# Kernel tuning notes

Hardware: AMD Instinct MI355X
Metric: run time of the kernel (lower is better)

Reference implementation:

```python
import jax, jax.numpy as jnp
import numpy as np

N_NODES = 100000
N_EDGES = 1600000
IN_F, HID, N_COLORS = 128, 128, 10


def setup_inputs() -> dict:
    key = jax.random.key(0)
    k1, k2, k3, k4 = jax.random.split(key, 4)
    x = jax.random.normal(k1, (N_NODES, IN_F), dtype=jnp.float32)
    edge_index = jax.random.randint(k2, (2, N_EDGES), 0, N_NODES, dtype=jnp.int64)
    # Glorot-ish init for weights
    W1 = jax.random.normal(k3, (IN_F, HID), dtype=jnp.float32) / np.sqrt(IN_F)
    b1 = jnp.zeros((HID,), dtype=jnp.float32)
    W2 = jax.random.normal(k4, (HID, N_COLORS), dtype=jnp.float32) / np.sqrt(HID)
    b2 = jnp.zeros((N_COLORS,), dtype=jnp.float32)
    return {"x": x, "edge_index": edge_index, "W1": W1, "b1": b1, "W2": W2, "b2": b2}


def _gcn_norm(edge_index, num_nodes):
    # Add self-loops, compute symmetric normalization D^-1/2 (A+I) D^-1/2
    loops = jnp.arange(num_nodes, dtype=edge_index.dtype)
    src = jnp.concatenate([edge_index[0], loops])
    dst = jnp.concatenate([edge_index[1], loops])
    deg = jax.ops.segment_sum(jnp.ones_like(dst, dtype=jnp.float32), dst,
                              num_segments=num_nodes)
    deg_isqrt = jax.lax.rsqrt(deg)  # deg >= 1 due to self-loops
    norm = deg_isqrt[src] * deg_isqrt[dst]  # [E + N]
    return src, dst, norm


def _gcn_conv(h, src, dst, norm, num_nodes, W, b):
    # Linear transform first (PyG GCNConv), then gather-scale-scatter aggregate
    h = h @ W                                   # [N, out]
    msg = h[src] * norm[:, None]                # [E + N, out] gather
    out = jax.ops.segment_sum(msg, dst, num_segments=num_nodes)  # scatter-add
    return out + b


def reference(x, edge_index, W1, b1, W2, b2):
    n = x.shape[0]
    src, dst, norm = _gcn_norm(edge_index, n)
    h = _gcn_conv(x, src, dst, norm, n, W1, b1)
    h = jax.nn.relu(h)
    # dropout is identity in eval mode
    h = _gcn_conv(h, src, dst, norm, n, W2, b2)
    return jax.nn.softmax(h, axis=1)
```

## Files before the change

### kernel.cpp

```cpp
#include <hip/hip_runtime.h>
#include <hip/hip_fp16.h>

#define IN_F 128
#define HID  128
#define NC   10
#define H2P  16
#define NPB  128
#define NBMAX 784
#define BCAP 2560
#define EPB  4096

typedef _Float16 f16x8 __attribute__((ext_vector_type(8)));
typedef float f32x4 __attribute__((ext_vector_type(4)));
typedef int int4a __attribute__((ext_vector_type(4), aligned(4)));

__device__ inline __half2 shfl_xor_h2(__half2 v, int mask) {
    int i = __shfl_xor(*reinterpret_cast<int*>(&v), mask, 64);
    return *reinterpret_cast<__half2*>(&i);
}

__global__ __launch_bounds__(1024) void k_bin(const int* __restrict__ src,
                                              const int* __restrict__ dst,
                                              int* __restrict__ bcnt,
                                              unsigned int* __restrict__ binned,
                                              const float* __restrict__ W1,
                                              __half* __restrict__ WT,
                                              int E, int nbin) {
    __shared__ int hist[NBMAX];
    __shared__ int base[NBMAX];
    __shared__ int lcur[NBMAX];
    const int tid = threadIdx.x;

    if (blockIdx.x == 0) {
        for (int i = tid; i < IN_F * HID; i += 1024) {
            int k = i >> 7, n = i & 127;
            WT[n * IN_F + k] = __float2half(W1[k * HID + n]);
        }
    }

    for (int b = tid; b < nbin; b += 1024) { hist[b] = 0; lcur[b] = 0; }
    __syncthreads();

    const int e0 = blockIdx.x * EPB + tid;
    int d[4];
    #pragma unroll
    for (int u = 0; u < 4; u++) {
        int e = e0 + u * 1024;
        d[u] = (e < E) ? dst[e] : -1;
        if (d[u] >= 0) atomicAdd(&hist[d[u] >> 7], 1);
    }
    __syncthreads();
    for (int b = tid; b < nbin; b += 1024) {
        int h = hist[b];
        base[b] = h ? atomicAdd(&bcnt[b], h) : 0;
    }
    __syncthreads();
    #pragma unroll
    for (int u = 0; u < 4; u++) {
        int e = e0 + u * 1024;
        if (e < E) {
            int dd = d[u];
            int b = dd >> 7;
            int s = src[e];
            int o = base[b] + atomicAdd(&lcur[b], 1);
            if (o < BCAP)
                binned[(size_t)b * BCAP + o] = ((unsigned)(dd & 127) << 17) | (unsigned)s;
        }
    }
}

__global__ __launch_bounds__(256) void k_place2(const int* __restrict__ bcnt,
                                                const unsigned int* __restrict__ binned,
                                                int* __restrict__ rowptr,
                                                float* __restrict__ dis,
                                                int* __restrict__ csr,
                                                int N, int E, int nbin) {
    __shared__ int h[NPB];
    __shared__ int lb[NPB];
    __shared__ int cur[NPB];
    __shared__ int red[256];
    const int b = blockIdx.x;
    const int tid = threadIdx.x;

    int partial = 0;
    for (int i = tid; i < b; i += 256) partial += bcnt[i];
    red[tid] = partial;
    if (tid < NPB) h[tid] = 0;
    __syncthreads();
    #pragma unroll
    for (int off = 128; off > 0; off >>= 1) {
        if (tid < off) red[tid] += red[tid + off];
        __syncthreads();
    }
    const int rb = red[0];

    const int m = min(bcnt[b], BCAP);
    const unsigned int* p = binned + (size_t)b * BCAP;
    for (int i = tid; i < m; i += 256) atomicAdd(&h[p[i] >> 17], 1);
    __syncthreads();
    if (tid < NPB) lb[tid] = h[tid];
    __syncthreads();
    #pragma unroll
    for (int off = 1; off < NPB; off <<= 1) {
        int t = (tid < NPB && tid >= off) ? lb[tid - off] : 0;
        __syncthreads();
        if (tid < NPB) lb[tid] += t;
        __syncthreads();
    }
    if (tid < NPB) {
        int ex = lb[tid] - h[tid];
        int node = b * NPB + tid;
        if (node < N) {
            rowptr[node] = rb + ex;
            dis[node] = rsqrtf(1.0f + (float)h[tid]);
        }
        lb[tid] = ex;
        cur[tid] = 0;
    }
    if (b == nbin - 1 && tid == 0) rowptr[N] = E;
    __syncthreads();
    for (int i = tid; i < m; i += 256) {
        unsigned v = p[i];
        int dl = v >> 17;
        int r = atomicAdd(&cur[dl], 1);
        csr[rb + lb[dl] + r] = (int)(v & 0x1FFFF);
    }
}

__global__ __launch_bounds__(256) void k_gemm1(const float* __restrict__ X,
                                               const __half* __restrict__ WT,
                                               const float* __restrict__ dis,
                                               __half* __restrict__ outh) {
    __shared__ _Float16 sX[32 * IN_F];
    __shared__ _Float16 sW[128 * IN_F];
    const int tid = threadIdx.x;
    const int row0 = blockIdx.x * 32;

    {
        int n = tid >> 1, part = tid & 1;
        const f16x8* src = (const f16x8*)(WT + n * IN_F + part * 64);
        f16x8* dst = (f16x8*)(sW + n * IN_F + part * 64);
        #pragma unroll
        for (int c = 0; c < 8; c++) dst[c] = src[c];
    }
    {
        int r = tid >> 3;
        int k0 = (tid & 7) * 16;
        const float* sp = X + (size_t)(row0 + r) * IN_F + k0;
        float4 f0 = *(const float4*)(sp);
        float4 f1 = *(const float4*)(sp + 4);
        float4 f2 = *(const float4*)(sp + 8);
        float4 f3 = *(const float4*)(sp + 12);
        f16x8 h0, h1;
        h0[0] = (_Float16)f0.x; h0[1] = (_Float16)f0.y;
        h0[2] = (_Float16)f0.z; h0[3] = (_Float16)f0.w;
        h0[4] = (_Float16)f1.x; h0[5] = (_Float16)f1.y;
        h0[6] = (_Float16)f1.z; h0[7] = (_Float16)f1.w;
        h1[0] = (_Float16)f2.x; h1[1] = (_Float16)f2.y;
        h1[2] = (_Float16)f2.z; h1[3] = (_Float16)f2.w;
        h1[4] = (_Float16)f3.x; h1[5] = (_Float16)f3.y;
        h1[6] = (_Float16)f3.z; h1[7] = (_Float16)f3.w;
        *(f16x8*)(sX + r * IN_F + k0) = h0;
        *(f16x8*)(sX + r * IN_F + k0 + 8) = h1;
    }
    __syncthreads();

    const int wave = tid >> 6;
    const int lane = tid & 63;
    const int quad = lane >> 4;
    const int l16 = lane & 15;
    const int nbase = wave * 32;

    f32x4 acc00 = {0,0,0,0}, acc01 = {0,0,0,0}, acc10 = {0,0,0,0}, acc11 = {0,0,0,0};

    #pragma unroll
    for (int kc = 0; kc < 4; kc++) {
        const int koff = kc * 32 + quad * 8;
        f16x8 a0 = *(const f16x8*)(sX + l16 * IN_F + koff);
        f16x8 a1 = *(const f16x8*)(sX + (16 + l16) * IN_F + koff);
        f16x8 b0 = *(const f16x8*)(sW + (nbase + l16) * IN_F + koff);
        f16x8 b1 = *(const f16x8*)(sW + (nbase + 16 + l16) * IN_F + koff);
        acc00 = __builtin_amdgcn_mfma_f32_16x16x32_f16(a0, b0, acc00, 0, 0, 0);
        acc01 = __builtin_amdgcn_mfma_f32_16x16x32_f16(a0, b1, acc01, 0, 0, 0);
        acc10 = __builtin_amdgcn_mfma_f32_16x16x32_f16(a1, b0, acc10, 0, 0, 0);
        acc11 = __builtin_amdgcn_mfma_f32_16x16x32_f16(a1, b1, acc11, 0, 0, 0);
    }

    #pragma unroll
    for (int r = 0; r < 4; r++) {
        {
            int row = row0 + quad * 4 + r;
            float d = dis[row];
            __half* o = outh + (size_t)row * HID + nbase + l16;
            o[0]  = __float2half(acc00[r] * d);
            o[16] = __float2half(acc01[r] * d);
        }
        {
            int row = row0 + 16 + quad * 4 + r;
            float d = dis[row];
            __half* o = outh + (size_t)row * HID + nbase + l16;
            o[0]  = __float2half(acc10[r] * d);
            o[16] = __float2half(acc11[r] * d);
        }
    }
}

__global__ __launch_bounds__(256) void k_agg1(const __half* __restrict__ hsh,
                                              const int* __restrict__ rowptr,
                                              const int* __restrict__ csr,
                                              const float* __restrict__ dis,
                                              const float* __restrict__ b1,
                                              const float* __restrict__ W2,
                                              __half* __restrict__ h2h,
                                              int N, int E) {
    __shared__ float sWT[NC][IN_F];
    for (int i = threadIdx.x; i < NC * IN_F; i += 256)
        sWT[i >> 7][i & 127] = W2[(i & 127) * NC + (i >> 7)];
    __syncthreads();

    const int node = blockIdx.x * 4 + (threadIdx.x >> 6);
    if (node >= N) return;
    const int lane = threadIdx.x & 63;
    const int g   = lane >> 4;
    const int l16 = lane & 15;
    const int f0  = l16 * 8;

    const int beg = rowptr[node], end = rowptr[node + 1];
    const __half2 hz = __half2half2(__float2half(0.0f));
    const __half2 ho = __half2half2(__float2half(1.0f));
    const unsigned nclamp = (unsigned)(N - 1);

    __half2 acc2[4] = {hz, hz, hz, hz};
    if (g == 0) {
        float4 r = *(const float4*)(hsh + (size_t)node * HID + f0);
        const __half2* hh = (const __half2*)&r;
        acc2[0] = hh[0]; acc2[1] = hh[1]; acc2[2] = hh[2]; acc2[3] = hh[3];
    }

    for (int j0 = beg + 4 * g; j0 < end; j0 += 16) {
        int bj = min(j0, E - 4);
        int off = j0 - bj;
        int rem = end - j0;
        int4a cv = *(const int4a*)(csr + bj);
        unsigned s0 = min((unsigned)cv[0], nclamp);
        unsigned s1 = min((unsigned)cv[1], nclamp);
        unsigned s2 = min((unsigned)cv[2], nclamp);
        unsigned s3 = min((unsigned)cv[3], nclamp);
        __half2 w0 = ((unsigned)(0 - off) < (unsigned)rem) ? ho : hz;
        __half2 w1 = ((unsigned)(1 - off) < (unsigned)rem) ? ho : hz;
        __half2 w2 = ((unsigned)(2 - off) < (unsigned)rem) ? ho : hz;
        __half2 w3 = ((unsigned)(3 - off) < (unsigned)rem) ? ho : hz;
        float4 r0 = *(const float4*)(hsh + (size_t)s0 * HID + f0);
        float4 r1 = *(const float4*)(hsh + (size_t)s1 * HID + f0);
        float4 r2 = *(const float4*)(hsh + (size_t)s2 * HID + f0);
        float4 r3 = *(const float4*)(hsh + (size_t)s3 * HID + f0);
        const __half2* h0 = (const __half2*)&r0;
        const __half2* h1 = (const __half2*)&r1;
        const __half2* h2 = (const __half2*)&r2;
        const __half2* h3 = (const __half2*)&r3;
        #pragma unroll
        for (int i = 0; i < 4; i++) {
            acc2[i] = __hfma2(w0, h0[i], acc2[i]);
            acc2[i] = __hfma2(w1, h1[i], acc2[i]);
            acc2[i] = __hfma2(w2, h2[i], acc2[i]);
            acc2[i] = __hfma2(w3, h3[i], acc2[i]);
        }
    }

    #pragma unroll
    for (int i = 0; i < 4; i++) {
        acc2[i] = __hadd2(acc2[i], shfl_xor_h2(acc2[i], 16));
        acc2[i] = __hadd2(acc2[i], shfl_xor_h2(acc2[i], 32));
    }
    float acc[8];
    #pragma unroll
    for (int i = 0; i < 4; i++) {
        float2 t = __half22float2(acc2[i]);
        acc[2 * i] = t.x; acc[2 * i + 1] = t.y;
    }

    const float d = dis[node];
    float4 ba = *(const float4*)(b1 + f0);
    float4 bb = *(const float4*)(b1 + f0 + 4);
    float h[8];
    h[0] = fmaxf(fmaf(d, acc[0], ba.x), 0.0f);
    h[1] = fmaxf(fmaf(d, acc[1], ba.y), 0.0f);
    h[2] = fmaxf(fmaf(d, acc[2], ba.z), 0.0f);
    h[3] = fmaxf(fmaf(d, acc[3], ba.w), 0.0f);
    h[4] = fmaxf(fmaf(d, acc[4], bb.x), 0.0f);
    h[5] = fmaxf(fmaf(d, acc[5], bb.y), 0.0f);
    h[6] = fmaxf(fmaf(d, acc[6], bb.z), 0.0f);
    h[7] = fmaxf(fmaf(d, acc[7], bb.w), 0.0f);

    const int cb = (g == 0) ? 0 : (g == 1) ? 3 : (g == 2) ? 6 : 8;
    const int nc = (g < 2) ? 3 : 2;
    float p[3];
    #pragma unroll
    for (int ci = 0; ci < 3; ci++) {
        if (ci < nc) {
            int c = cb + ci;
            float4 wa = *(const float4*)&sWT[c][f0];
            float4 wb = *(const float4*)&sWT[c][f0 + 4];
            float t = fmaf(h[0], wa.x, fmaf(h[1], wa.y, fmaf(h[2], wa.z, h[3] * wa.w)));
            t = fmaf(h[4], wb.x, fmaf(h[5], wb.y, fmaf(h[6], wb.z, fmaf(h[7], wb.w, t))));
            #pragma unroll
            for (int off = 1; off < 16; off <<= 1) t += __shfl_xor(t, off, 64);
            p[ci] = t;
        }
    }
    if (l16 == 0) {
        __half* o = h2h + (size_t)node * H2P + cb;
        for (int ci = 0; ci < nc; ci++) o[ci] = __float2half(d * p[ci]);
    }
}

__global__ __launch_bounds__(256) void k_agg2(const __half* __restrict__ h2h,
                                              const int* __restrict__ rowptr,
                                              const int* __restrict__ csr,
                                              const float* __restrict__ dis,
                                              const float* __restrict__ b2,
                                              float* __restrict__ out,
                                              int N, int E) {
    int t = blockIdx.x * 256 + threadIdx.x;
    int node = t >> 1;
    int q = t & 1;
    if (node >= N) return;
    const int base = q * 8;
    const __half2 hz = __half2half2(__float2half(0.0f));
    const __half2 ho = __half2half2(__float2half(1.0f));
    const unsigned nclamp = (unsigned)(N - 1);

    __half2 a2[4];
    {
        float4 r = *(const float4*)(h2h + (size_t)node * H2P + base);
        const __half2* hh = (const __half2*)&r;
        a2[0] = hh[0]; a2[1] = hh[1]; a2[2] = hh[2]; a2[3] = hh[3];
    }
    const int beg = rowptr[node], end = rowptr[node + 1];
    for (int j0 = beg; j0 < end; j0 += 4) {
        int bj = min(j0, E - 4);
        int off = j0 - bj;
        int rem = end - j0;
        int4a cv = *(const int4a*)(csr + bj);
        unsigned s0 = min((unsigned)cv[0], nclamp);
        unsigned s1 = min((unsigned)cv[1], nclamp);
        unsigned s2 = min((unsigned)cv[2], nclamp);
        unsigned s3 = min((unsigned)cv[3], nclamp);
        __half2 w0 = ((unsigned)(0 - off) < (unsigned)rem) ? ho : hz;
        __half2 w1 = ((unsigned)(1 - off) < (unsigned)rem) ? ho : hz;
        __half2 w2 = ((unsigned)(2 - off) < (unsigned)rem) ? ho : hz;
        __half2 w3 = ((unsigned)(3 - off) < (unsigned)rem) ? ho : hz;
        float4 r0 = *(const float4*)(h2h + (size_t)s0 * H2P + base);
        float4 r1 = *(const float4*)(h2h + (size_t)s1 * H2P + base);
        float4 r2 = *(const float4*)(h2h + (size_t)s2 * H2P + base);
        float4 r3 = *(const float4*)(h2h + (size_t)s3 * H2P + base);
        const __half2* h0 = (const __half2*)&r0;
        const __half2* h1 = (const __half2*)&r1;
        const __half2* h2 = (const __half2*)&r2;
        const __half2* h3 = (const __half2*)&r3;
        #pragma unroll
        for (int i = 0; i < 4; i++) {
            a2[i] = __hfma2(w0, h0[i], a2[i]);
            a2[i] = __hfma2(w1, h1[i], a2[i]);
            a2[i] = __hfma2(w2, h2[i], a2[i]);
            a2[i] = __hfma2(w3, h3[i], a2[i]);
        }
    }

    float a[8];
    #pragma unroll
    for (int i = 0; i < 4; i++) {
        float2 tt = __half22float2(a2[i]);
        a[2 * i] = tt.x; a[2 * i + 1] = tt.y;
    }

    const float d = dis[node];
    float vv[8];
    #pragma unroll
    for (int i = 0; i < 8; i++) {
        int f = base + i;
        vv[i] = (f < NC) ? fmaf(d, a[i], b2[f]) : -1e30f;
    }
    float m = vv[0];
    #pragma unroll
    for (int i = 1; i < 8; i++) m = fmaxf(m, vv[i]);
    m = fmaxf(m, __shfl_xor(m, 1, 64));
    float e[8];
    float s = 0.0f;
    #pragma unroll
    for (int i = 0; i < 8; i++) { e[i] = (base + i < NC) ? expf(vv[i] - m) : 0.0f; s += e[i]; }
    s += __shfl_xor(s, 1, 64);
    float inv = 1.0f / s;

    float* o = out + (size_t)node * NC;
    if (q == 0) {
        *(float2*)(o + 0) = make_float2(e[0] * inv, e[1] * inv);
        *(float2*)(o + 2) = make_float2(e[2] * inv, e[3] * inv);
        *(float2*)(o + 4) = make_float2(e[4] * inv, e[5] * inv);
        *(float2*)(o + 6) = make_float2(e[6] * inv, e[7] * inv);
    } else {
        *(float2*)(o + 8) = make_float2(e[0] * inv, e[1] * inv);
    }
}

extern "C" void kernel_launch(void* const* d_in, const int* in_sizes, int n_in,
                              void* d_out, int out_size, void* d_ws, size_t ws_size,
                              hipStream_t stream) {
    const float* x  = (const float*)d_in[0];
    const int*   ei = (const int*)d_in[1];
    const float* W1 = (const float*)d_in[2];
    const float* b1 = (const float*)d_in[3];
    const float* W2 = (const float*)d_in[4];
    const float* b2 = (const float*)d_in[5];
    float* out = (float*)d_out;

    const int N = in_sizes[0] / IN_F;
    const int E = in_sizes[1] / 2;
    const int* esrc = ei;
    const int* edst = ei + E;
    const int nbin = (N + NPB - 1) / NPB;

    char* ws = (char*)d_ws;
    int*    rowptr  = (int*)(ws);
    float*  dis     = (float*)(ws + 0x80000);
    int*    bcnt    = (int*)(ws + 0x100000);
    __half* WT      = (__half*)(ws + 0x110000);
    unsigned int* binned = (unsigned int*)(ws + 0x140000);
    int*    csr     = (int*)(ws + 0x940000);
    __half* hsh     = (__half*)(ws + 0x1040000);
    __half* h2h     = (__half*)(ws + 0x2A00000);

    hipMemsetAsync(bcnt, 0, (size_t)nbin * sizeof(int), stream);

    k_bin   <<<(E + EPB - 1) / EPB, 1024, 0, stream>>>(esrc, edst, bcnt, binned, W1, WT, E, nbin);
    k_place2<<<nbin, 256, 0, stream>>>(bcnt, binned, rowptr, dis, csr, N, E, nbin);
    k_gemm1 <<<N / 32, 256, 0, stream>>>(x, WT, dis, hsh);
    k_agg1  <<<(N + 3) / 4, 256, 0, stream>>>(hsh, rowptr, csr, dis, b1, W2, h2h, N, E);
    k_agg2  <<<(int)(((size_t)N * 2 + 255) / 256), 256, 0, stream>>>(h2h, rowptr, csr, dis, b2, out, N, E);
}
```

Before: 252.0 us.

## Fuse CSR placement with GEMM1, pad rows to multiples of four, parallelize agg2

The CSR placement kernel and the first GEMM are merged into one kernel per 128-node bin, which removes a launch and the serial per-block prefix sum over bin counts. Each node's edge list is padded to a multiple of four with a dummy index that points to a zeroed row, stored at fixed per-bin offsets (CAPP) and described by a (start, count) pair. This lets both aggregation loops drop the boundary masking and index clamping and use plain adds. W2 is transposed once up front, and agg2 now uses 8 threads per node with a shuffle reduction instead of 2. The fused kernel has much larger shared memory and fewer blocks, and the padding plus fixed bin capacity add slightly more gather traffic and a layout assumption about per-bin edge counts.

```diff
diff --git a/kernel.cpp b/kernel.cpp
--- a/kernel.cpp
+++ b/kernel.cpp
@@ -8,6 +8,7 @@
 #define NPB  128
 #define NBMAX 784
 #define BCAP 2560
+#define CAPP 2944
 #define EPB  4096
 
 typedef _Float16 f16x8 __attribute__((ext_vector_type(8)));
@@ -25,6 +26,8 @@
                                               unsigned int* __restrict__ binned,
                                               const float* __restrict__ W1,
                                               __half* __restrict__ WT,
+                                              const float* __restrict__ W2,
+                                              float* __restrict__ W2T,
                                               int E, int nbin) {
     __shared__ int hist[NBMAX];
     __shared__ int base[NBMAX];
@@ -36,6 +39,8 @@
             int k = i >> 7, n = i & 127;
             WT[n * IN_F + k] = __float2half(W1[k * HID + n]);
         }
+        for (int i = tid; i < NC * IN_F; i += 1024)
+            W2T[i] = W2[(i & 127) * NC + (i >> 7)];
     }
 
     for (int b = tid; b < nbin; b += 1024) { hist[b] = 0; lcur[b] = 0; }
@@ -69,36 +74,35 @@
     }
 }
 
-__global__ __launch_bounds__(256) void k_place2(const int* __restrict__ bcnt,
-                                                const unsigned int* __restrict__ binned,
-                                                int* __restrict__ rowptr,
-                                                float* __restrict__ dis,
-                                                int* __restrict__ csr,
-                                                int N, int E, int nbin) {
+__global__ __launch_bounds__(256) void k_pg(const int* __restrict__ bcnt,
+                                            const unsigned int* __restrict__ binned,
+                                            int2* __restrict__ rowinfo,
+                                            float* __restrict__ dis,
+                                            int* __restrict__ csr,
+                                            const float* __restrict__ X,
+                                            const __half* __restrict__ WT,
+                                            __half* __restrict__ hsh,
+                                            __half* __restrict__ h2h,
+                                            int N) {
     __shared__ int h[NPB];
     __shared__ int lb[NPB];
     __shared__ int cur[NPB];
-    __shared__ int red[256];
+    __shared__ float sdis[NPB];
+    __shared__ _Float16 sX[32 * IN_F];
+    __shared__ _Float16 sW[128 * IN_F];
     const int b = blockIdx.x;
     const int tid = threadIdx.x;
 
-    int partial = 0;
-    for (int i = tid; i < b; i += 256) partial += bcnt[i];
-    red[tid] = partial;
     if (tid < NPB) h[tid] = 0;
     __syncthreads();
-    #pragma unroll
-    for (int off = 128; off > 0; off >>= 1) {
-        if (tid < off) red[tid] += red[tid + off];
-        __syncthreads();
-    }
-    const int rb = red[0];
 
     const int m = min(bcnt[b], BCAP);
     const unsigned int* p = binned + (size_t)b * BCAP;
     for (int i = tid; i < m; i += 256) atomicAdd(&h[p[i] >> 17], 1);
     __syncthreads();
-    if (tid < NPB) lb[tid] = h[tid];
+
+    int myh = 0, cnt4 = 0;
+    if (tid < NPB) { myh = h[tid]; cnt4 = (myh + 3) & ~3; lb[tid] = cnt4; }
     __syncthreads();
     #pragma unroll
     for (int off = 1; off < NPB; off <<= 1) {
@@ -107,115 +111,118 @@
         if (tid < NPB) lb[tid] += t;
         __syncthreads();
     }
+    int ex = 0;
     if (tid < NPB) {
-        int ex = lb[tid] - h[tid];
+        ex = lb[tid] - cnt4;
         int node = b * NPB + tid;
         if (node < N) {
-            rowptr[node] = rb + ex;
-            dis[node] = rsqrtf(1.0f + (float)h[tid]);
+            rowinfo[node] = make_int2(b * CAPP + ex, cnt4);
+            float dd = rsqrtf(1.0f + (float)myh);
+            dis[node] = dd;
+            sdis[tid] = dd;
         }
         lb[tid] = ex;
         cur[tid] = 0;
     }
-    if (b == nbin - 1 && tid == 0) rowptr[N] = E;
     __syncthreads();
     for (int i = tid; i < m; i += 256) {
         unsigned v = p[i];
         int dl = v >> 17;
         int r = atomicAdd(&cur[dl], 1);
-        csr[rb + lb[dl] + r] = (int)(v & 0x1FFFF);
-    }
-}
-
-__global__ __launch_bounds__(256) void k_gemm1(const float* __restrict__ X,
-                                               const __half* __restrict__ WT,
-                                               const float* __restrict__ dis,
-                                               __half* __restrict__ outh) {
-    __shared__ _Float16 sX[32 * IN_F];
-    __shared__ _Float16 sW[128 * IN_F];
-    const int tid = threadIdx.x;
-    const int row0 = blockIdx.x * 32;
+        csr[b * CAPP + lb[dl] + r] = (int)(v & 0x1FFFF);
+    }
+    if (tid < NPB) {
+        for (int k = myh; k < cnt4; k++) csr[b * CAPP + ex + k] = N;
+    }
+    if (b == 0) {
+        f16x8 z = {0, 0, 0, 0, 0, 0, 0, 0};
+        if (tid < 16) *(f16x8*)(hsh + (size_t)N * HID + tid * 8) = z;
+        if (tid < 2)  *(f16x8*)(h2h + (size_t)N * H2P + tid * 8) = z;
+    }
 
     {
         int n = tid >> 1, part = tid & 1;
-        const f16x8* src = (const f16x8*)(WT + n * IN_F + part * 64);
-        f16x8* dst = (f16x8*)(sW + n * IN_F + part * 64);
+        const f16x8* srcp = (const f16x8*)(WT + n * IN_F + part * 64);
+        f16x8* dstp = (f16x8*)(sW + n * IN_F + part * 64);
         #pragma unroll
-        for (int c = 0; c < 8; c++) dst[c] = src[c];
-    }
-    {
-        int r = tid >> 3;
-        int k0 = (tid & 7) * 16;
-        const float* sp = X + (size_t)(row0 + r) * IN_F + k0;
-        float4 f0 = *(const float4*)(sp);
-        float4 f1 = *(const float4*)(sp + 4);
-        float4 f2 = *(const float4*)(sp + 8);
-        float4 f3 = *(const float4*)(sp + 12);
-        f16x8 h0, h1;
-        h0[0] = (_Float16)f0.x; h0[1] = (_Float16)f0.y;
-        h0[2] = (_Float16)f0.z; h0[3] = (_Float16)f0.w;
-        h0[4] = (_Float16)f1.x; h0[5] = (_Float16)f1.y;
-        h0[6] = (_Float16)f1.z; h0[7] = (_Float16)f1.w;
-        h1[0] = (_Float16)f2.x; h1[1] = (_Float16)f2.y;
-        h1[2] = (_Float16)f2.z; h1[3] = (_Float16)f2.w;
-        h1[4] = (_Float16)f3.x; h1[5] = (_Float16)f3.y;
-        h1[6] = (_Float16)f3.z; h1[7] = (_Float16)f3.w;
-        *(f16x8*)(sX + r * IN_F + k0) = h0;
-        *(f16x8*)(sX + r * IN_F + k0 + 8) = h1;
-    }
-    __syncthreads();
-
+        for (int c = 0; c < 8; c++) dstp[c] = srcp[c];
+    }
     const int wave = tid >> 6;
     const int lane = tid & 63;
     const int quad = lane >> 4;
     const int l16 = lane & 15;
     const int nbase = wave * 32;
 
-    f32x4 acc00 = {0,0,0,0}, acc01 = {0,0,0,0}, acc10 = {0,0,0,0}, acc11 = {0,0,0,0};
-
-    #pragma unroll
-    for (int kc = 0; kc < 4; kc++) {
-        const int koff = kc * 32 + quad * 8;
-        f16x8 a0 = *(const f16x8*)(sX + l16 * IN_F + koff);
-        f16x8 a1 = *(const f16x8*)(sX + (16 + l16) * IN_F + koff);
-        f16x8 b0 = *(const f16x8*)(sW + (nbase + l16) * IN_F + koff);
-        f16x8 b1 = *(const f16x8*)(sW + (nbase + 16 + l16) * IN_F + koff);
-        acc00 = __builtin_amdgcn_mfma_f32_16x16x32_f16(a0, b0, acc00, 0, 0, 0);
-        acc01 = __builtin_amdgcn_mfma_f32_16x16x32_f16(a0, b1, acc01, 0, 0, 0);
-        acc10 = __builtin_amdgcn_mfma_f32_16x16x32_f16(a1, b0, acc10, 0, 0, 0);
-        acc11 = __builtin_amdgcn_mfma_f32_16x16x32_f16(a1, b1, acc11, 0, 0, 0);
-    }
-
-    #pragma unroll
-    for (int r = 0; r < 4; r++) {
+    for (int tdx = 0; tdx < 4; tdx++) {
+        int row0 = b * NPB + tdx * 32;
+        if (row0 >= N) break;
+        __syncthreads();
         {
-            int row = row0 + quad * 4 + r;
-            float d = dis[row];
-            __half* o = outh + (size_t)row * HID + nbase + l16;
-            o[0]  = __float2half(acc00[r] * d);
-            o[16] = __float2half(acc01[r] * d);
-        }
-        {
-            int row = row0 + 16 + quad * 4 + r;
-            float d = dis[row];
-            __half* o = outh + (size_t)row * HID + nbase + l16;
-            o[0]  = __float2half(acc10[r] * d);
-            o[16] = __float2half(acc11[r] * d);
+            int r = tid >> 3;
+            int k0 = (tid & 7) * 16;
+            const float* sp = X + (size_t)(row0 + r) * IN_F + k0;
+            float4 f0 = *(const float4*)(sp);
+            float4 f1 = *(const float4*)(sp + 4);
+            float4 f2 = *(const float4*)(sp + 8);
+            float4 f3 = *(const float4*)(sp + 12);
+            f16x8 h0, h1;
+            h0[0] = (_Float16)f0.x; h0[1] = (_Float16)f0.y;
+            h0[2] = (_Float16)f0.z; h0[3] = (_Float16)f0.w;
+            h0[4] = (_Float16)f1.x; h0[5] = (_Float16)f1.y;
+            h0[6] = (_Float16)f1.z; h0[7] = (_Float16)f1.w;
+            h1[0] = (_Float16)f2.x; h1[1] = (_Float16)f2.y;
+            h1[2] = (_Float16)f2.z; h1[3] = (_Float16)f2.w;
+            h1[4] = (_Float16)f3.x; h1[5] = (_Float16)f3.y;
+            h1[6] = (_Float16)f3.z; h1[7] = (_Float16)f3.w;
+            *(f16x8*)(sX + r * IN_F + k0) = h0;
+            *(f16x8*)(sX + r * IN_F + k0 + 8) = h1;
+        }
+        __syncthreads();
+
+        f32x4 acc00 = {0,0,0,0}, acc01 = {0,0,0,0}, acc10 = {0,0,0,0}, acc11 = {0,0,0,0};
+        #pragma unroll
+        for (int kc = 0; kc < 4; kc++) {
+            const int koff = kc * 32 + quad * 8;
+            f16x8 a0 = *(const f16x8*)(sX + l16 * IN_F + koff);
+            f16x8 a1 = *(const f16x8*)(sX + (16 + l16) * IN_F + koff);
+            f16x8 b0 = *(const f16x8*)(sW + (nbase + l16) * IN_F + koff);
+            f16x8 b1 = *(const f16x8*)(sW + (nbase + 16 + l16) * IN_F + koff);
+            acc00 = __builtin_amdgcn_mfma_f32_16x16x32_f16(a0, b0, acc00, 0, 0, 0);
+            acc01 = __builtin_amdgcn_mfma_f32_16x16x32_f16(a0, b1, acc01, 0, 0, 0);
+            acc10 = __builtin_amdgcn_mfma_f32_16x16x32_f16(a1, b0, acc10, 0, 0, 0);
+            acc11 = __builtin_amdgcn_mfma_f32_16x16x32_f16(a1, b1, acc11, 0, 0, 0);
+        }
+        #pragma unroll
+        for (int r = 0; r < 4; r++) {
+            {
+                int lr = tdx * 32 + quad * 4 + r;
+                float d = sdis[lr];
+                __half* o = hsh + (size_t)(b * NPB + lr) * HID + nbase + l16;
+                o[0]  = __float2half(acc00[r] * d);
+                o[16] = __float2half(acc01[r] * d);
+            }
+            {
+                int lr = tdx * 32 + 16 + quad * 4 + r;
+                float d = sdis[lr];
+                __half* o = hsh + (size_t)(b * NPB + lr) * HID + nbase + l16;
+                o[0]  = __float2half(acc10[r] * d);
+                o[16] = __float2half(acc11[r] * d);
+            }
         }
     }
 }
 
 __global__ __launch_bounds__(256) void k_agg1(const __half* __restrict__ hsh,
-                                              const int* __restrict__ rowptr,
+                                              const int2* __restrict__ rowinfo,
                                               const int* __restrict__ csr,
                                               const float* __restrict__ dis,
                                               const float* __restrict__ b1,
-                                              const float* __restrict__ W2,
+                                              const float* __restrict__ W2T,
                                               __half* __restrict__ h2h,
-                                              int N, int E) {
+                                              int N) {
     __shared__ float sWT[NC][IN_F];
     for (int i = threadIdx.x; i < NC * IN_F; i += 256)
-        sWT[i >> 7][i & 127] = W2[(i & 127) * NC + (i >> 7)];
+        ((float*)sWT)[i] = W2T[i];
     __syncthreads();
 
     const int node = blockIdx.x * 4 + (threadIdx.x >> 6);
@@ -224,11 +231,10 @@
     const int g   = lane >> 4;
     const int l16 = lane & 15;
     const int f0  = l16 * 8;
-
-    const int beg = rowptr[node], end = rowptr[node + 1];
     const __half2 hz = __half2half2(__float2half(0.0f));
-    const __half2 ho = __half2half2(__float2half(1.0f));
-    const unsigned nclamp = (unsigned)(N - 1);
+
+    const int2 ri = rowinfo[node];
+    const int beg = ri.x, end = ri.x + ri.y;
 
     __half2 acc2[4] = {hz, hz, hz, hz};
     if (g == 0) {
@@ -238,32 +244,21 @@
     }
 
     for (int j0 = beg + 4 * g; j0 < end; j0 += 16) {
-        int bj = min(j0, E - 4);
-        int off = j0 - bj;
-        int rem = end - j0;
-        int4a cv = *(const int4a*)(csr + bj);
-        unsigned s0 = min((unsigned)cv[0], nclamp);
-        unsigned s1 = min((unsigned)cv[1], nclamp);
-        unsigned s2 = min((unsigned)cv[2], nclamp);
-        unsigned s3 = min((unsigned)cv[3], nclamp);
-        __half2 w0 = ((unsigned)(0 - off) < (unsigned)rem) ? ho : hz;
-        __half2 w1 = ((unsigned)(1 - off) < (unsigned)rem) ? ho : hz;
-        __half2 w2 = ((unsigned)(2 - off) < (unsigned)rem) ? ho : hz;
-        __half2 w3 = ((unsigned)(3 - off) < (unsigned)rem) ? ho : hz;
-        float4 r0 = *(const float4*)(hsh + (size_t)s0 * HID + f0);
-        float4 r1 = *(const float4*)(hsh + (size_t)s1 * HID + f0);
-        float4 r2 = *(const float4*)(hsh + (size_t)s2 * HID + f0);
-        float4 r3 = *(const float4*)(hsh + (size_t)s3 * HID + f0);
+        int4a cv = *(const int4a*)(csr + j0);
+        float4 r0 = *(const float4*)(hsh + (size_t)cv[0] * HID + f0);
+        float4 r1 = *(const float4*)(hsh + (size_t)cv[1] * HID + f0);
+        float4 r2 = *(const float4*)(hsh + (size_t)cv[2] * HID + f0);
+        float4 r3 = *(const float4*)(hsh + (size_t)cv[3] * HID + f0);
         const __half2* h0 = (const __half2*)&r0;
         const __half2* h1 = (const __half2*)&r1;
         const __half2* h2 = (const __half2*)&r2;
         const __half2* h3 = (const __half2*)&r3;
         #pragma unroll
         for (int i = 0; i < 4; i++) {
-            acc2[i] = __hfma2(w0, h0[i], acc2[i]);
-            acc2[i] = __hfma2(w1, h1[i], acc2[i]);
-            acc2[i] = __hfma2(w2, h2[i], acc2[i]);
-            acc2[i] = __hfma2(w3, h3[i], acc2[i]);
+            acc2[i] = __hadd2(acc2[i], h0[i]);
+            acc2[i] = __hadd2(acc2[i], h1[i]);
+            acc2[i] = __hadd2(acc2[i], h2[i]);
+            acc2[i] = __hadd2(acc2[i], h3[i]);
         }
     }
 
@@ -315,56 +310,52 @@
 }
 
 __global__ __launch_bounds__(256) void k_agg2(const __half* __restrict__ h2h,
-                                              const int* __restrict__ rowptr,
+                                              const int2* __restrict__ rowinfo,
                                               const int* __restrict__ csr,
                                               const float* __restrict__ dis,
                                               const float* __restrict__ b2,
                                               float* __restrict__ out,
-                                              int N, int E) {
+                                              int N) {
     int t = blockIdx.x * 256 + threadIdx.x;
-    int node = t >> 1;
-    int q = t & 1;
+    int node = t >> 3;
     if (node >= N) return;
+    int o = t & 7;
+    int q = o & 1;
+    int eg = o >> 1;
     const int base = q * 8;
     const __half2 hz = __half2half2(__float2half(0.0f));
-    const __half2 ho = __half2half2(__float2half(1.0f));
-    const unsigned nclamp = (unsigned)(N - 1);
-
-    __half2 a2[4];
-    {
+
+    __half2 a2[4] = {hz, hz, hz, hz};
+    if (eg == 0) {
         float4 r = *(const float4*)(h2h + (size_t)node * H2P + base);
         const __half2* hh = (const __half2*)&r;
         a2[0] = hh[0]; a2[1] = hh[1]; a2[2] = hh[2]; a2[3] = hh[3];
     }
-    const int beg = rowptr[node], end = rowptr[node + 1];
-    for (int j0 = beg; j0 < end; j0 += 4) {
-        int bj = min(j0, E - 4);
-        int off = j0 - bj;
-        int rem = end - j0;
-        int4a cv = *(const int4a*)(csr + bj);
-        unsigned s0 = min((unsigned)cv[0], nclamp);
-        unsigned s1 = min((unsigned)cv[1], nclamp);
-        unsigned s2 = min((unsigned)cv[2], nclamp);
-        unsigned s3 = min((unsigned)cv[3], nclamp);
-        __half2 w0 = ((unsigned)(0 - off) < (unsigned)rem) ? ho : hz;
-        __half2 w1 = ((unsigned)(1 - off) < (unsigned)rem) ? ho : hz;
-        __half2 w2 = ((unsigned)(2 - off) < (unsigned)rem) ? ho : hz;
-        __half2 w3 = ((unsigned)(3 - off) < (unsigned)rem) ? ho : hz;
-        float4 r0 = *(const float4*)(h2h + (size_t)s0 * H2P + base);
-        float4 r1 = *(const float4*)(h2h + (size_t)s1 * H2P + base);
-        float4 r2 = *(const float4*)(h2h + (size_t)s2 * H2P + base);
-        float4 r3 = *(const float4*)(h2h + (size_t)s3 * H2P + base);
+    const int2 ri = rowinfo[node];
+    const int end = ri.x + ri.y;
+    for (int j0 = ri.x + 4 * eg; j0 < end; j0 += 16) {
+        int4a cv = *(const int4a*)(csr + j0);
+        float4 r0 = *(const float4*)(h2h + (size_t)cv[0] * H2P + base);
+        float4 r1 = *(const float4*)(h2h + (size_t)cv[1] * H2P + base);
+        float4 r2 = *(const float4*)(h2h + (size_t)cv[2] * H2P + base);
+        float4 r3 = *(const float4*)(h2h + (size_t)cv[3] * H2P + base);
         const __half2* h0 = (const __half2*)&r0;
         const __half2* h1 = (const __half2*)&r1;
         const __half2* h2 = (const __half2*)&r2;
         const __half2* h3 = (const __half2*)&r3;
         #pragma unroll
         for (int i = 0; i < 4; i++) {
-            a2[i] = __hfma2(w0, h0[i], a2[i]);
-            a2[i] = __hfma2(w1, h1[i], a2[i]);
-            a2[i] = __hfma2(w2, h2[i], a2[i]);
-            a2[i] = __hfma2(w3, h3[i], a2[i]);
-        }
+            a2[i] = __hadd2(a2[i], h0[i]);
+            a2[i] = __hadd2(a2[i], h1[i]);
+            a2[i] = __hadd2(a2[i], h2[i]);
+            a2[i] = __hadd2(a2[i], h3[i]);
+        }
+    }
+
+    #pragma unroll
+    for (int i = 0; i < 4; i++) {
+        a2[i] = __hadd2(a2[i], shfl_xor_h2(a2[i], 2));
+        a2[i] = __hadd2(a2[i], shfl_xor_h2(a2[i], 4));
     }
 
     float a[8];
@@ -392,14 +383,14 @@
     s += __shfl_xor(s, 1, 64);
     float inv = 1.0f / s;
 
-    float* o = out + (size_t)node * NC;
-    if (q == 0) {
-        *(float2*)(o + 0) = make_float2(e[0] * inv, e[1] * inv);
-        *(float2*)(o + 2) = make_float2(e[2] * inv, e[3] * inv);
-        *(float2*)(o + 4) = make_float2(e[4] * inv, e[5] * inv);
-        *(float2*)(o + 6) = make_float2(e[6] * inv, e[7] * inv);
-    } else {
-        *(float2*)(o + 8) = make_float2(e[0] * inv, e[1] * inv);
+    float* op = out + (size_t)node * NC;
+    if (o == 0) {
+        *(float2*)(op + 0) = make_float2(e[0] * inv, e[1] * inv);
+        *(float2*)(op + 2) = make_float2(e[2] * inv, e[3] * inv);
+        *(float2*)(op + 4) = make_float2(e[4] * inv, e[5] * inv);
+        *(float2*)(op + 6) = make_float2(e[6] * inv, e[7] * inv);
+    } else if (o == 1) {
+        *(float2*)(op + 8) = make_float2(e[0] * inv, e[1] * inv);
     }
 }
 
@@ -421,20 +412,20 @@
     const int nbin = (N + NPB - 1) / NPB;
 
     char* ws = (char*)d_ws;
-    int*    rowptr  = (int*)(ws);
-    float*  dis     = (float*)(ws + 0x80000);
-    int*    bcnt    = (int*)(ws + 0x100000);
-    __half* WT      = (__half*)(ws + 0x110000);
-    unsigned int* binned = (unsigned int*)(ws + 0x140000);
-    int*    csr     = (int*)(ws + 0x940000);
-    __half* hsh     = (__half*)(ws + 0x1040000);
-    __half* h2h     = (__half*)(ws + 0x2A00000);
+    int2*   rowinfo = (int2*)(ws);
+    float*  dis     = (float*)(ws + 0x100000);
+    int*    bcnt    = (int*)(ws + 0x180000);
+    __half* WT      = (__half*)(ws + 0x190000);
+    float*  W2T     = (float*)(ws + 0x1A0000);
+    unsigned int* binned = (unsigned int*)(ws + 0x200000);
+    int*    csr     = (int*)(ws + 0xA00000);
+    __half* hsh     = (__half*)(ws + 0x1400000);
+    __half* h2h     = (__half*)(ws + 0x2D00000);
 
     hipMemsetAsync(bcnt, 0, (size_t)nbin * sizeof(int), stream);
 
-    k_bin   <<<(E + EPB - 1) / EPB, 1024, 0, stream>>>(esrc, edst, bcnt, binned, W1, WT, E, nbin);
-    k_place2<<<nbin, 256, 0, stream>>>(bcnt, binned, rowptr, dis, csr, N, E, nbin);
-    k_gemm1 <<<N / 32, 256, 0, stream>>>(x, WT, dis, hsh);
-    k_agg1  <<<(N + 3) / 4, 256, 0, stream>>>(hsh, rowptr, csr, dis, b1, W2, h2h, N, E);
-    k_agg2  <<<(int)(((size_t)N * 2 + 255) / 256), 256, 0, stream>>>(h2h, rowptr, csr, dis, b2, out, N, E);
-}
+    k_bin <<<(E + EPB - 1) / EPB, 1024, 0, stream>>>(esrc, edst, bcnt, binned, W1, WT, W2, W2T, E, nbin);
+    k_pg  <<<nbin, 256, 0, stream>>>(bcnt, binned, rowinfo, dis, csr, x, WT, hsh, h2h, N);
+    k_agg1<<<(N + 3) / 4, 256, 0, stream>>>(hsh, rowinfo, csr, dis, b1, W2T, h2h, N);
+    k_agg2<<<(int)(((size_t)N * 8 + 255) / 256), 256, 0, stream>>>(h2h, rowinfo, csr, dis, b2, out, N);
+}
```

Result: faster. 245.8 us (-2.5%).
